# Performance work log

Measured on AMD Instinct MI355X. Metric: run time of the kernel, lower is better.

Reference implementation:

```python
import jax, jax.numpy as jnp
import numpy as np

AMOUNT = 0.02  # skimage random_noise(mode='s&p', amount=0.02), salt_vs_pepper=0.5


def setup_inputs() -> dict:
    key = jax.random.key(0)
    k1, k2 = jax.random.split(key)
    B, C, H, W = 64, 3, 512, 512
    noised_image = jax.random.uniform(k1, (B, C, H, W), dtype=jnp.float32)
    noise_u = jax.random.uniform(k2, (B, C, H, W), dtype=jnp.float32)
    return {"noised_image": noised_image, "noise_u": noise_u}


def reference(noised_image, noise_u):
    # salt & pepper: fraction AMOUNT of pixels flipped; half -> pepper (0.0), half -> salt (1.0)
    half = jnp.asarray(AMOUNT * 0.5, noised_image.dtype)
    full = jnp.asarray(AMOUNT, noised_image.dtype)
    out = jnp.where(
        noise_u < half,
        jnp.asarray(0.0, noised_image.dtype),
        jnp.where(noise_u < full, jnp.asarray(1.0, noised_image.dtype), noised_image),
    )
    return out
```

## Files before the change

kernel.cpp:

```cpp
#include <hip/hip_runtime.h>


#define HALF_T 0.01f
#define FULL_T 0.02f

typedef float floatx4 __attribute__((ext_vector_type(4)));

__device__ __forceinline__ floatx4 sp_select(floatx4 uv, floatx4 iv) {
    floatx4 ov;
    ov.x = (uv.x < HALF_T) ? 0.0f : (uv.x < FULL_T) ? 1.0f : iv.x;
    ov.y = (uv.y < HALF_T) ? 0.0f : (uv.y < FULL_T) ? 1.0f : iv.y;
    ov.z = (uv.z < HALF_T) ? 0.0f : (uv.z < FULL_T) ? 1.0f : iv.z;
    ov.w = (uv.w < HALF_T) ? 0.0f : (uv.w < FULL_T) ? 1.0f : iv.w;
    return ov;
}

__global__ __launch_bounds__(256) void saltpepper_x4_kernel(
    const floatx4* __restrict__ img,
    const floatx4* __restrict__ u,
    floatx4* __restrict__ out)
{
    int base = blockIdx.x * 1024 + threadIdx.x;

    floatx4 u0 = u[base];
    floatx4 u1 = u[base + 256];
    floatx4 u2 = u[base + 512];
    floatx4 u3 = u[base + 768];
    floatx4 i0 = img[base];
    floatx4 i1 = img[base + 256];
    floatx4 i2 = img[base + 512];
    floatx4 i3 = img[base + 768];

    floatx4 o0 = sp_select(u0, i0);
    floatx4 o1 = sp_select(u1, i1);
    floatx4 o2 = sp_select(u2, i2);
    floatx4 o3 = sp_select(u3, i3);

    __builtin_nontemporal_store(o0, &out[base]);
    __builtin_nontemporal_store(o1, &out[base + 256]);
    __builtin_nontemporal_store(o2, &out[base + 512]);
    __builtin_nontemporal_store(o3, &out[base + 768]);
}

__global__ __launch_bounds__(256) void saltpepper_f4_tail_kernel(
    const floatx4* __restrict__ img,
    const floatx4* __restrict__ u,
    floatx4* __restrict__ out,
    int start4, int n4)
{
    int i = start4 + blockIdx.x * blockDim.x + threadIdx.x;
    if (i < n4) {
        out[i] = sp_select(u[i], img[i]);
    }
}

__global__ __launch_bounds__(256) void saltpepper_scalar_tail_kernel(
    const float* __restrict__ img,
    const float* __restrict__ u,
    float* __restrict__ out,
    int start, int n)
{
    int i = start + blockIdx.x * blockDim.x + threadIdx.x;
    if (i < n) {
        float uv = u[i];
        out[i] = (uv < HALF_T) ? 0.0f : (uv < FULL_T) ? 1.0f : img[i];
    }
}

extern "C" void kernel_launch(void* const* d_in, const int* in_sizes, int n_in,
                              void* d_out, int out_size, void* d_ws, size_t ws_size,
                              hipStream_t stream) {
    const float* img = (const float*)d_in[0];
    const float* u   = (const float*)d_in[1];
    float* out = (float*)d_out;
    int n = in_sizes[0];

    int n4 = n / 4;
    int nb = n4 / 1024;
    int f4_done = nb * 1024;
    int sc_done = n4 * 4;

    if (nb > 0) {
        saltpepper_x4_kernel<<<nb, 256, 0, stream>>>(
            (const floatx4*)img, (const floatx4*)u, (floatx4*)out);
    }
    int f4_tail = n4 - f4_done;
    if (f4_tail > 0) {
        int g = (f4_tail + 255) / 256;
        saltpepper_f4_tail_kernel<<<g, 256, 0, stream>>>(
            (const floatx4*)img, (const floatx4*)u, (floatx4*)out, f4_done, n4);
    }
    int sc_tail = n - sc_done;
    if (sc_tail > 0) {
        int g = (sc_tail + 255) / 256;
        saltpepper_scalar_tail_kernel<<<g, 256, 0, stream>>>(
            img, u, out, sc_done, n);
    }
}
```

Before: 444.7 us.

## Add persistent-style software-pipelined kernel prefetching next chunk during stores

Introduces a kernel where each of up to 2048 blocks processes several 1024-vector chunks, loading the next chunk's inputs into registers before computing and storing the current one. The intent is to keep more memory requests in flight per thread and reduce block launch overhead, improving bandwidth utilization. The old one-chunk kernel is kept for the remaining chunks. Register use rises and the reduced grid may lower parallelism.

```diff
diff --git a/kernel.cpp b/kernel.cpp
--- a/kernel.cpp
+++ b/kernel.cpp
@@ -3,6 +3,8 @@
 
 #define HALF_T 0.01f
 #define FULL_T 0.02f
+#define TPB 256
+#define CHUNK (4 * TPB)
 
 typedef float floatx4 __attribute__((ext_vector_type(4)));
 
@@ -15,12 +17,52 @@
     return ov;
 }
 
+__global__ __launch_bounds__(256) void saltpepper_pipe_kernel(
+    const floatx4* __restrict__ img,
+    const floatx4* __restrict__ u,
+    floatx4* __restrict__ out,
+    int cpb)
+{
+    int base = blockIdx.x * cpb * CHUNK + threadIdx.x;
+
+    floatx4 ua[4], ia[4], ub[4], ib[4];
+
+#pragma unroll
+    for (int j = 0; j < 4; ++j) ua[j] = u[base + j * TPB];
+#pragma unroll
+    for (int j = 0; j < 4; ++j) ia[j] = img[base + j * TPB];
+
+    for (int k = 0; k < cpb - 1; ++k) {
+        int nbase = base + CHUNK;
+#pragma unroll
+        for (int j = 0; j < 4; ++j) ub[j] = u[nbase + j * TPB];
+#pragma unroll
+        for (int j = 0; j < 4; ++j) ib[j] = img[nbase + j * TPB];
+
+#pragma unroll
+        for (int j = 0; j < 4; ++j) {
+            __builtin_nontemporal_store(sp_select(ua[j], ia[j]),
+                                        &out[base + j * TPB]);
+        }
+#pragma unroll
+        for (int j = 0; j < 4; ++j) { ua[j] = ub[j]; ia[j] = ib[j]; }
+        base = nbase;
+    }
+
+#pragma unroll
+    for (int j = 0; j < 4; ++j) {
+        __builtin_nontemporal_store(sp_select(ua[j], ia[j]),
+                                    &out[base + j * TPB]);
+    }
+}
+
 __global__ __launch_bounds__(256) void saltpepper_x4_kernel(
     const floatx4* __restrict__ img,
     const floatx4* __restrict__ u,
-    floatx4* __restrict__ out)
+    floatx4* __restrict__ out,
+    int chunk0)
 {
-    int base = blockIdx.x * 1024 + threadIdx.x;
+    int base = (chunk0 + blockIdx.x) * CHUNK + threadIdx.x;
 
     floatx4 u0 = u[base];
     floatx4 u1 = u[base + 256];
@@ -31,15 +73,10 @@
     floatx4 i2 = img[base + 512];
     floatx4 i3 = img[base + 768];
 
-    floatx4 o0 = sp_select(u0, i0);
-    floatx4 o1 = sp_select(u1, i1);
-    floatx4 o2 = sp_select(u2, i2);
-    floatx4 o3 = sp_select(u3, i3);
-
-    __builtin_nontemporal_store(o0, &out[base]);
-    __builtin_nontemporal_store(o1, &out[base + 256]);
-    __builtin_nontemporal_store(o2, &out[base + 512]);
-    __builtin_nontemporal_store(o3, &out[base + 768]);
+    __builtin_nontemporal_store(sp_select(u0, i0), &out[base]);
+    __builtin_nontemporal_store(sp_select(u1, i1), &out[base + 256]);
+    __builtin_nontemporal_store(sp_select(u2, i2), &out[base + 512]);
+    __builtin_nontemporal_store(sp_select(u3, i3), &out[base + 768]);
 }
 
 __global__ __launch_bounds__(256) void saltpepper_f4_tail_kernel(
@@ -76,20 +113,34 @@
     int n = in_sizes[0];
 
     int n4 = n / 4;
-    int nb = n4 / 1024;
-    int f4_done = nb * 1024;
-    int sc_done = n4 * 4;
+    int nchunks = n4 / CHUNK;
 
-    if (nb > 0) {
-        saltpepper_x4_kernel<<<nb, 256, 0, stream>>>(
-            (const floatx4*)img, (const floatx4*)u, (floatx4*)out);
+    int done_chunks = 0;
+    if (nchunks > 0) {
+        int NB = nchunks >= 2048 ? 2048 : nchunks;
+        int cpb = nchunks / NB;
+        saltpepper_pipe_kernel<<<NB, 256, 0, stream>>>(
+            (const floatx4*)img, (const floatx4*)u, (floatx4*)out, cpb);
+        done_chunks = NB * cpb;
+
+        int rem_chunks = nchunks - done_chunks;
+        if (rem_chunks > 0) {
+            saltpepper_x4_kernel<<<rem_chunks, 256, 0, stream>>>(
+                (const floatx4*)img, (const floatx4*)u, (floatx4*)out,
+                done_chunks);
+            done_chunks = nchunks;
+        }
     }
+
+    int f4_done = done_chunks * CHUNK;
     int f4_tail = n4 - f4_done;
     if (f4_tail > 0) {
         int g = (f4_tail + 255) / 256;
         saltpepper_f4_tail_kernel<<<g, 256, 0, stream>>>(
             (const floatx4*)img, (const floatx4*)u, (floatx4*)out, f4_done, n4);
     }
+
+    int sc_done = n4 * 4;
     int sc_tail = n - sc_done;
     if (sc_tail > 0) {
         int g = (sc_tail + 255) / 256;
```

Measured after the change: 458.9 us. 3.2% more time.
